# Optimization experiments

Hardware: AMD Instinct MI355X
Metric: run time of the kernel (lower is better)

Reference implementation:

```python
import jax, jax.numpy as jnp
import numpy as np

B, L, D = 8, 8192, 768  # trees, leaves per tree, d_in == d_hidden


def setup_inputs() -> dict:
    key = jax.random.key(0)
    ks = jax.random.split(key, 5)
    scale = 0.02  # keep gates out of saturation
    return {
        "leaf_emb": jax.random.normal(ks[0], (B, L, D), dtype=jnp.float32),
        "W_iou": jax.random.normal(ks[1], (3 * D, D), dtype=jnp.float32) * scale,
        "b_iou": jnp.zeros((3 * D,), dtype=jnp.float32),
        "U_iou": jax.random.normal(ks[2], (3 * D, D), dtype=jnp.float32) * scale,
        "W_f": jax.random.normal(ks[3], (D, D), dtype=jnp.float32) * scale,
        "b_f": jnp.zeros((D,), dtype=jnp.float32),
        "U_f": jax.random.normal(ks[4], (D, D), dtype=jnp.float32) * scale,
    }


def reference(leaf_emb, W_iou, b_iou, U_iou, W_f, b_f, U_f):
    """Child-Sum Tree-LSTM over a perfect binary tree, level-synchronous.

    Leaves: h = embedding, c = 0 (matches the torch module's leaf case).
    Internal node with children (l, r):
      h_sum = h_l + h_r; x = h_sum / 2
      i,o,u = split(W_iou x + b_iou + U_iou h_sum)
      f_k   = sigmoid(W_f x + b_f + U_f h_k)   per child
      c = sigmoid(i)*tanh(u) + f_l*c_l + f_r*c_r;  h = sigmoid(o)*tanh(c)
    Returns stacked (h_root, c_root): [2, B, D].
    """
    h = leaf_emb                      # [B, n, D]
    c = jnp.zeros_like(h)
    while h.shape[1] > 1:             # static trace-time loop over depth (13 levels)
        hl, hr = h[:, 0::2], h[:, 1::2]   # [B, n/2, D]
        cl, cr = c[:, 0::2], c[:, 1::2]
        h_sum = hl + hr
        x = h_sum * 0.5               # x_j = h_sum / num_children (==2)
        iou = jnp.einsum('bnd,gd->bng', x, W_iou) + b_iou \
            + jnp.einsum('bnd,gd->bng', h_sum, U_iou)
        i, o, u = jnp.split(iou, 3, axis=-1)
        wfx = jnp.einsum('bnd,hd->bnh', x, W_f) + b_f
        f_l = jax.nn.sigmoid(wfx + jnp.einsum('bnd,hd->bnh', hl, U_f))
        f_r = jax.nn.sigmoid(wfx + jnp.einsum('bnd,hd->bnh', hr, U_f))
        c = jax.nn.sigmoid(i) * jnp.tanh(u) + f_l * cl + f_r * cr
        h = jax.nn.sigmoid(o) * jnp.tanh(c)
    return jnp.stack([h[:, 0], c[:, 0]])  # [2, B, D]
```

## Files before the change

kernel.cpp:

```cpp
#include <hip/hip_runtime.h>


typedef _Float16 half8 __attribute__((ext_vector_type(8)));
typedef float f32x4 __attribute__((ext_vector_type(4)));

#define ROWB 1536
#define NT 24
#define BUFA 36864
#define BUFT 26624

__device__ __forceinline__ float sigm(float x){ return 1.f/(1.f+__expf(-x)); }
__device__ __forceinline__ float tanhfast(float x){ return 1.f - 2.f/(1.f+__expf(2.f*x)); }

__device__ __forceinline__ void gload16(const void* g, void* l){
  __builtin_amdgcn_global_load_lds((const __attribute__((address_space(1))) void*)g,
                                   (__attribute__((address_space(3))) void*)l, 16, 0, 0);
}

__global__ void prep_weights(const float* __restrict__ Wiou, const float* __restrict__ Uiou,
                             const float* __restrict__ Wf, const float* __restrict__ Uf,
                             _Float16* __restrict__ Bw)
{
    const int n1 = 2304 * 768, n2 = n1 + 589824, n3 = n2 + 589824;
    int stride = gridDim.x * blockDim.x;
    for (int idx = blockIdx.x * blockDim.x + threadIdx.x; idx < n3; idx += stride) {
        float v;
        if (idx < n1)      v = __fmaf_rn(0.5f, Wiou[idx], Uiou[idx]);
        else if (idx < n2) v = 0.5f * Wf[idx - n1];
        else               v = Uf[idx - n2];
        Bw[idx] = (_Float16)v;
    }
}

__global__ void cast_leaves(const float* __restrict__ x, _Float16* __restrict__ h, int n8)
{
    int stride = gridDim.x * blockDim.x;
    for (int i = blockIdx.x * blockDim.x + threadIdx.x; i < n8; i += stride) {
        float4 v0 = ((const float4*)x)[2 * i];
        float4 v1 = ((const float4*)x)[2 * i + 1];
        half8 o = { (_Float16)v0.x, (_Float16)v0.y, (_Float16)v0.z, (_Float16)v0.w,
                    (_Float16)v1.x, (_Float16)v1.y, (_Float16)v1.z, (_Float16)v1.w };
        ((half8*)h)[i] = o;
    }
}

__global__ __launch_bounds__(256, 2) void tree_level(
    const _Float16* __restrict__ Hc, const float* __restrict__ Cc,
    const _Float16* __restrict__ Bw,
    const float* __restrict__ biou, const float* __restrict__ bfv,
    _Float16* __restrict__ Hn, float* __restrict__ Cn,
    int M, int mblocks, int firstLevel)
{
    __shared__ __align__(16) char smem[2 * BUFA];
    const int tid = threadIdx.x;
    const int lane = tid & 63;
    const int w = tid >> 6;
    const int wm = w >> 1;
    const int wd = w & 1;

    const int nwg = mblocks * 12;
    const int orig = blockIdx.x;
    const int xcd = orig & 7, qx = nwg >> 3, rx = nwg & 7;
    const int v = (xcd < rx ? xcd * (qx + 1) : rx * (qx + 1) + (xcd - rx) * qx) + (orig >> 3);
    const int mb = v / 12;
    const int d0c = v - mb * 12;
    const int mBase = mb * 128;
    const int d0 = d0c * 64;

    const int l3 = lane >> 3, j = lane & 7;
    const int jjA = j ^ l3;
    const int rbase = w * 8 + l3;
    unsigned offH[4];
#pragma unroll
    for (int s = 0; s < 4; ++s)
        offH[s] = (unsigned)(2 * (mBase + s * 32 + rbase) + (jjA >> 2)) * ROWB + (jjA & 3) * 16;
    const int pB = w * 8 + l3;
    unsigned offWb[5];
#pragma unroll
    for (int t = 0; t < 5; ++t)
        offWb[t] = (unsigned)(t * 768 + d0 + 2 * pB + (jjA >> 2)) * ROWB + (jjA & 3) * 16;
    const int wK = w * 1024;

#define STAGE_A(bi, ko) do { \
    _Pragma("unroll") for (int s = 0; s < 4; ++s) \
        gload16((const char*)Hc + offH[s] + (ko), smem + (bi) * BUFA + s * 4096 + wK); \
    _Pragma("unroll") for (int t = 0; t < 5; ++t) \
        gload16((const char*)Bw + offWb[t] + (ko), smem + (bi) * BUFA + 16384 + t * 4096 + wK); \
} while (0)

    const int q = lane >> 4;
    const int lr16 = lane & 15;
    int offA[4], offB[2];
#pragma unroll
    for (int fm = 0; fm < 4; ++fm) {
        int r = wm * 64 + fm * 16 + lr16;
        offA[fm] = r * 128 + ((q ^ (r & 7)) * 16);
    }
#pragma unroll
    for (int fd = 0; fd < 2; ++fd) {
        int cl = wd * 32 + fd * 16 + lr16;
        int p = cl >> 1;
        int jb = ((cl & 1) * 4 + q) ^ (p & 7);
        offB[fd] = 16384 + p * 128 + jb * 16;
    }

    f32x4 acc[6][4][2];
#pragma unroll
    for (int g = 0; g < 6; ++g)
#pragma unroll
        for (int a = 0; a < 4; ++a)
#pragma unroll
            for (int b2 = 0; b2 < 2; ++b2)
                acc[g][a][b2] = (f32x4){0.f, 0.f, 0.f, 0.f};

    STAGE_A(0, 0);
    int cur = 0;
    for (int kt = 0; kt < NT; ++kt) {
        if (kt + 1 < NT) {
            STAGE_A(cur ^ 1, (kt + 1) * 64);
            asm volatile("s_waitcnt vmcnt(9)" ::: "memory");
        } else {
            asm volatile("s_waitcnt vmcnt(0)" ::: "memory");
        }
        __builtin_amdgcn_s_barrier();
        __builtin_amdgcn_sched_barrier(0);
        const char* bb = smem + cur * BUFA;
        half8 hl[4], hr[4];
#pragma unroll
        for (int fm = 0; fm < 4; ++fm) {
            hl[fm] = *(const half8*)(bb + offA[fm]);
            hr[fm] = *(const half8*)(bb + (offA[fm] ^ 64));
        }
        __builtin_amdgcn_s_setprio(1);
#pragma unroll
        for (int fd = 0; fd < 2; ++fd) {
            const char* bp = bb + offB[fd];
            half8 b0 = *(const half8*)(bp);
            half8 b1 = *(const half8*)(bp + 4096);
            half8 b2 = *(const half8*)(bp + 8192);
            half8 b3 = *(const half8*)(bp + 12288);
            half8 b4 = *(const half8*)(bp + 16384);
#pragma unroll
            for (int fm = 0; fm < 4; ++fm) {
                acc[4][fm][fd] = __builtin_amdgcn_mfma_f32_16x16x32_f16(hl[fm], b4, acc[4][fm][fd], 0, 0, 0);
                half8 hs = hl[fm] + hr[fm];
                acc[0][fm][fd] = __builtin_amdgcn_mfma_f32_16x16x32_f16(hs, b0, acc[0][fm][fd], 0, 0, 0);
                acc[1][fm][fd] = __builtin_amdgcn_mfma_f32_16x16x32_f16(hs, b1, acc[1][fm][fd], 0, 0, 0);
                acc[2][fm][fd] = __builtin_amdgcn_mfma_f32_16x16x32_f16(hs, b2, acc[2][fm][fd], 0, 0, 0);
                acc[3][fm][fd] = __builtin_amdgcn_mfma_f32_16x16x32_f16(hs, b3, acc[3][fm][fd], 0, 0, 0);
                acc[5][fm][fd] = __builtin_amdgcn_mfma_f32_16x16x32_f16(hs, b4, acc[5][fm][fd], 0, 0, 0);
            }
        }
        __builtin_amdgcn_s_setprio(0);
        if (kt + 1 < NT) __builtin_amdgcn_s_barrier();
        cur ^= 1;
    }

#pragma unroll
    for (int fd = 0; fd < 2; ++fd) {
        const int col = d0 + wd * 32 + fd * 16 + lr16;
        const float bi = biou[col];
        const float bo = biou[768 + col];
        const float bu = biou[1536 + col];
        const float bf = bfv[col];
#pragma unroll
        for (int fm = 0; fm < 4; ++fm) {
            const int rb = mBase + wm * 64 + fm * 16 + q * 4;
#pragma unroll
            for (int r4 = 0; r4 < 4; ++r4) {
                int row = rb + r4;
                float iv = acc[0][fm][fd][r4] + bi;
                float ov = acc[1][fm][fd][r4] + bo;
                float uv = acc[2][fm][fd][r4] + bu;
                float wfx = acc[3][fm][fd][r4] + bf;
                float g6 = acc[4][fm][fd][r4];
                float fl = sigm(wfx + g6);
                float fr = sigm(wfx + acc[5][fm][fd][r4] - g6);
                float clv = 0.f, crv = 0.f;
                if (!firstLevel) {
                    clv = Cc[(size_t)(2 * row) * 768 + col];
                    crv = Cc[(size_t)(2 * row + 1) * 768 + col];
                }
                float c = sigm(iv) * tanhfast(uv) + fl * clv + fr * crv;
                float h = sigm(ov) * tanhfast(c);
                Hn[(size_t)row * 768 + col] = (_Float16)h;
                Cn[(size_t)row * 768 + col] = c;
            }
        }
    }
}

__global__ __launch_bounds__(256, 3) void tree_small(
    const _Float16* __restrict__ Hc, const float* __restrict__ Cc,
    const _Float16* __restrict__ Bw,
    const float* __restrict__ biou, const float* __restrict__ bfv,
    _Float16* __restrict__ Hn, float* __restrict__ Cn,
    float* __restrict__ out,
    int M, int finalLevel)
{
    __shared__ __align__(16) char smem[2 * BUFT];
    const int tid = threadIdx.x;
    const int lane = tid & 63;
    const int w = tid >> 6;
    const int wm = w >> 1;
    const int wd = w & 1;
    const int bid = blockIdx.x;
    const int mb = bid / 24;
    const int d0c = bid - mb * 24;
    const int mBase = mb * 128;
    const int d0 = d0c * 32;

    const int l3 = lane >> 3, j = lane & 7;
    const int jj0 = j ^ l3;

    unsigned offWb[3];
    int dstB[3];
#pragma unroll
    for (int s = 0; s < 3; ++s) {
        int i = s * 4 + w;
        if (i >= 10) i -= 2;
        int t = i >> 1, half = i & 1;
        int p = half * 8 + l3;
        offWb[s] = (unsigned)(t * 768 + d0 + 2 * p + (jj0 >> 2)) * ROWB + (jj0 & 3) * 16;
        dstB[s] = 16384 + t * 2048 + half * 1024;
    }
    unsigned offHa[4];
    int dstA[4];
#pragma unroll
    for (int s = 0; s < 4; ++s) {
        int u = s * 4 + w;
        int gr = mBase + u * 8 + l3;
        if (gr >= M) gr = M - 1;
        offHa[s] = (unsigned)(2 * gr + (jj0 >> 2)) * ROWB + (jj0 & 3) * 16;
        dstA[s] = u * 1024;
    }

#define STAGE_T(bi_, ko) do { \
    _Pragma("unroll") for (int s = 0; s < 4; ++s) \
        gload16((const char*)Hc + offHa[s] + (ko), smem + (bi_) * BUFT + dstA[s]); \
    _Pragma("unroll") for (int s = 0; s < 3; ++s) \
        gload16((const char*)Bw + offWb[s] + (ko), smem + (bi_) * BUFT + dstB[s]); \
} while (0)

    const int q = lane >> 4;
    const int lr16 = lane & 15;
    int offA[4];
#pragma unroll
    for (int fm = 0; fm < 4; ++fm) {
        int r = wm * 64 + fm * 16 + lr16;
        offA[fm] = r * 128 + ((q ^ (r & 7)) * 16);
    }
    int offB;
    {
        int cl = wd * 16 + lr16;
        int p = cl >> 1;
        int jb = ((cl & 1) * 4 + q) ^ (p & 7);
        offB = 16384 + p * 128 + jb * 16;
    }

    f32x4 acc[6][4];
#pragma unroll
    for (int g = 0; g < 6; ++g)
#pragma unroll
        for (int a = 0; a < 4; ++a)
            acc[g][a] = (f32x4){0.f, 0.f, 0.f, 0.f};

    STAGE_T(0, 0);
    int cur = 0;
    for (int kt = 0; kt < NT; ++kt) {
        if (kt + 1 < NT) {
            STAGE_T(cur ^ 1, (kt + 1) * 64);
            asm volatile("s_waitcnt vmcnt(7)" ::: "memory");
        } else {
            asm volatile("s_waitcnt vmcnt(0)" ::: "memory");
        }
        __builtin_amdgcn_s_barrier();
        __builtin_amdgcn_sched_barrier(0);
        const char* bb = smem + cur * BUFT;
        half8 b0 = *(const half8*)(bb + offB);
        half8 b1 = *(const half8*)(bb + offB + 2048);
        half8 b2 = *(const half8*)(bb + offB + 4096);
        half8 b3 = *(const half8*)(bb + offB + 6144);
        half8 b4 = *(const half8*)(bb + offB + 8192);
        __builtin_amdgcn_s_setprio(1);
#pragma unroll
        for (int fm = 0; fm < 4; ++fm) {
            half8 hl = *(const half8*)(bb + offA[fm]);
            half8 hr = *(const half8*)(bb + (offA[fm] ^ 64));
            acc[4][fm] = __builtin_amdgcn_mfma_f32_16x16x32_f16(hl, b4, acc[4][fm], 0, 0, 0);
            half8 hs = hl + hr;
            acc[0][fm] = __builtin_amdgcn_mfma_f32_16x16x32_f16(hs, b0, acc[0][fm], 0, 0, 0);
            acc[1][fm] = __builtin_amdgcn_mfma_f32_16x16x32_f16(hs, b1, acc[1][fm], 0, 0, 0);
            acc[2][fm] = __builtin_amdgcn_mfma_f32_16x16x32_f16(hs, b2, acc[2][fm], 0, 0, 0);
            acc[3][fm] = __builtin_amdgcn_mfma_f32_16x16x32_f16(hs, b3, acc[3][fm], 0, 0, 0);
            acc[5][fm] = __builtin_amdgcn_mfma_f32_16x16x32_f16(hs, b4, acc[5][fm], 0, 0, 0);
        }
        __builtin_amdgcn_s_setprio(0);
        if (kt + 1 < NT) __builtin_amdgcn_s_barrier();
        cur ^= 1;
    }

    const int col = d0 + wd * 16 + lr16;
    const float bi = biou[col];
    const float bo = biou[768 + col];
    const float bu = biou[1536 + col];
    const float bf = bfv[col];
#pragma unroll
    for (int fm = 0; fm < 4; ++fm) {
        const int rb = mBase + wm * 64 + fm * 16 + q * 4;
#pragma unroll
        for (int r4 = 0; r4 < 4; ++r4) {
            int row = rb + r4;
            if (row < M) {
                float iv = acc[0][fm][r4] + bi;
                float ov = acc[1][fm][r4] + bo;
                float uv = acc[2][fm][r4] + bu;
                float wfx = acc[3][fm][r4] + bf;
                float g6 = acc[4][fm][r4];
                float fl = sigm(wfx + g6);
                float fr = sigm(wfx + acc[5][fm][r4] - g6);
                float clv = Cc[(size_t)(2 * row) * 768 + col];
                float crv = Cc[(size_t)(2 * row + 1) * 768 + col];
                float c = sigm(iv) * tanhfast(uv) + fl * clv + fr * crv;
                float h = sigm(ov) * tanhfast(c);
                if (finalLevel) {
                    out[row * 768 + col] = h;
                    out[6144 + row * 768 + col] = c;
                } else {
                    Hn[(size_t)row * 768 + col] = (_Float16)h;
                    Cn[(size_t)row * 768 + col] = c;
                }
            }
        }
    }
}

extern "C" void kernel_launch(void* const* d_in, const int* in_sizes, int n_in,
                              void* d_out, int out_size, void* d_ws, size_t ws_size,
                              hipStream_t stream)
{
    const float* leaf = (const float*)d_in[0];
    const float* Wiou = (const float*)d_in[1];
    const float* biou = (const float*)d_in[2];
    const float* Uiou = (const float*)d_in[3];
    const float* Wf   = (const float*)d_in[4];
    const float* bfv  = (const float*)d_in[5];
    const float* Uf   = (const float*)d_in[6];

    char* ws = (char*)d_ws;
    _Float16* Bw = (_Float16*)(ws);
    _Float16* H0 = (_Float16*)(ws + 5898240);
    _Float16* H1 = (_Float16*)(ws + 106561536);
    float*    C0 = (float*)(ws + 156893184);
    float*    C1 = (float*)(ws + 257556480);

    prep_weights<<<1024, 256, 0, stream>>>(Wiou, Uiou, Wf, Uf, Bw);
    cast_leaves<<<2048, 256, 0, stream>>>(leaf, H0, 50331648 / 8);

    float* out = (float*)d_out;
    _Float16* Hc = H0; _Float16* Hn = H1;
    float* Cc = C1; float* Cn = C0;
    int rows = 65536, level = 0;
    while (rows > 8) {
        int M = rows >> 1;
        if (M >= 4096) {
            int mblocks = M / 128;
            tree_level<<<mblocks * 12, 256, 0, stream>>>(Hc, Cc, Bw, biou, bfv,
                Hn, Cn, M, mblocks, level == 0 ? 1 : 0);
        } else {
            int mblocks = (M + 127) / 128;
            int fin = (M == 8) ? 1 : 0;
            tree_small<<<mblocks * 24, 256, 0, stream>>>(Hc, Cc, Bw, biou, bfv,
                Hn, Cn, out, M, fin);
        }
        _Float16* th = Hc; Hc = Hn; Hn = th;
        float* tc = Cc; Cc = Cn; Cn = tc;
        rows = M; ++level;
    }
}
```

Measured before the change: 1.074 ms.

## Reformulate forget-gate GEMMs and fuse tail levels into persistent grid-synced kernel

The forget-gate weights are re-packed so each child's gate comes out of two MFMAs on hl and hr (0.5Wf+Uf and 0.5Wf) accumulated into one register set. This drops one accumulator group and one sum step in the epilogue, though each k-step now issues seven MFMAs per fragment instead of six. The small levels (M≤2048) now run in a single persistent 256-block kernel that separates levels with a global atomic barrier, replacing the per-level launches. Row bounds guards are also added to the big-level kernel. The persistent kernel relies on all 256 blocks being resident at once, or the spin barrier deadlocks.

```diff
diff --git a/kernel.cpp b/kernel.cpp
--- a/kernel.cpp
+++ b/kernel.cpp
@@ -19,15 +19,16 @@
 
 __global__ void prep_weights(const float* __restrict__ Wiou, const float* __restrict__ Uiou,
                              const float* __restrict__ Wf, const float* __restrict__ Uf,
-                             _Float16* __restrict__ Bw)
+                             _Float16* __restrict__ Bw, unsigned* __restrict__ barCnt)
 {
+    if (blockIdx.x == 0 && threadIdx.x == 0) atomicExch(barCnt, 0u);
     const int n1 = 2304 * 768, n2 = n1 + 589824, n3 = n2 + 589824;
     int stride = gridDim.x * blockDim.x;
     for (int idx = blockIdx.x * blockDim.x + threadIdx.x; idx < n3; idx += stride) {
         float v;
         if (idx < n1)      v = __fmaf_rn(0.5f, Wiou[idx], Uiou[idx]);
-        else if (idx < n2) v = 0.5f * Wf[idx - n1];
-        else               v = Uf[idx - n2];
+        else if (idx < n2) { int k = idx - n1; v = __fmaf_rn(0.5f, Wf[k], Uf[k]); }
+        else               { int k = idx - n2; v = 0.5f * Wf[k]; }
         Bw[idx] = (_Float16)v;
     }
 }
@@ -72,8 +73,11 @@
     const int rbase = w * 8 + l3;
     unsigned offH[4];
 #pragma unroll
-    for (int s = 0; s < 4; ++s)
-        offH[s] = (unsigned)(2 * (mBase + s * 32 + rbase) + (jjA >> 2)) * ROWB + (jjA & 3) * 16;
+    for (int s = 0; s < 4; ++s) {
+        int gr = mBase + s * 32 + rbase;
+        if (gr >= M) gr = M - 1;
+        offH[s] = (unsigned)(2 * gr + (jjA >> 2)) * ROWB + (jjA & 3) * 16;
+    }
     const int pB = w * 8 + l3;
     unsigned offWb[5];
 #pragma unroll
@@ -104,9 +108,9 @@
         offB[fd] = 16384 + p * 128 + jb * 16;
     }
 
-    f32x4 acc[6][4][2];
-#pragma unroll
-    for (int g = 0; g < 6; ++g)
+    f32x4 acc[5][4][2];
+#pragma unroll
+    for (int g = 0; g < 5; ++g)
 #pragma unroll
         for (int a = 0; a < 4; ++a)
 #pragma unroll
@@ -142,13 +146,14 @@
             half8 b4 = *(const half8*)(bp + 16384);
 #pragma unroll
             for (int fm = 0; fm < 4; ++fm) {
-                acc[4][fm][fd] = __builtin_amdgcn_mfma_f32_16x16x32_f16(hl[fm], b4, acc[4][fm][fd], 0, 0, 0);
                 half8 hs = hl[fm] + hr[fm];
                 acc[0][fm][fd] = __builtin_amdgcn_mfma_f32_16x16x32_f16(hs, b0, acc[0][fm][fd], 0, 0, 0);
                 acc[1][fm][fd] = __builtin_amdgcn_mfma_f32_16x16x32_f16(hs, b1, acc[1][fm][fd], 0, 0, 0);
                 acc[2][fm][fd] = __builtin_amdgcn_mfma_f32_16x16x32_f16(hs, b2, acc[2][fm][fd], 0, 0, 0);
-                acc[3][fm][fd] = __builtin_amdgcn_mfma_f32_16x16x32_f16(hs, b3, acc[3][fm][fd], 0, 0, 0);
-                acc[5][fm][fd] = __builtin_amdgcn_mfma_f32_16x16x32_f16(hs, b4, acc[5][fm][fd], 0, 0, 0);
+                acc[3][fm][fd] = __builtin_amdgcn_mfma_f32_16x16x32_f16(hl[fm], b3, acc[3][fm][fd], 0, 0, 0);
+                acc[3][fm][fd] = __builtin_amdgcn_mfma_f32_16x16x32_f16(hr[fm], b4, acc[3][fm][fd], 0, 0, 0);
+                acc[4][fm][fd] = __builtin_amdgcn_mfma_f32_16x16x32_f16(hl[fm], b4, acc[4][fm][fd], 0, 0, 0);
+                acc[4][fm][fd] = __builtin_amdgcn_mfma_f32_16x16x32_f16(hr[fm], b3, acc[4][fm][fd], 0, 0, 0);
             }
         }
         __builtin_amdgcn_s_setprio(0);
@@ -169,34 +174,33 @@
 #pragma unroll
             for (int r4 = 0; r4 < 4; ++r4) {
                 int row = rb + r4;
-                float iv = acc[0][fm][fd][r4] + bi;
-                float ov = acc[1][fm][fd][r4] + bo;
-                float uv = acc[2][fm][fd][r4] + bu;
-                float wfx = acc[3][fm][fd][r4] + bf;
-                float g6 = acc[4][fm][fd][r4];
-                float fl = sigm(wfx + g6);
-                float fr = sigm(wfx + acc[5][fm][fd][r4] - g6);
-                float clv = 0.f, crv = 0.f;
-                if (!firstLevel) {
-                    clv = Cc[(size_t)(2 * row) * 768 + col];
-                    crv = Cc[(size_t)(2 * row + 1) * 768 + col];
+                if (row < M) {
+                    float iv = acc[0][fm][fd][r4] + bi;
+                    float ov = acc[1][fm][fd][r4] + bo;
+                    float uv = acc[2][fm][fd][r4] + bu;
+                    float fl = sigm(acc[3][fm][fd][r4] + bf);
+                    float fr = sigm(acc[4][fm][fd][r4] + bf);
+                    float clv = 0.f, crv = 0.f;
+                    if (!firstLevel) {
+                        clv = Cc[(size_t)(2 * row) * 768 + col];
+                        crv = Cc[(size_t)(2 * row + 1) * 768 + col];
+                    }
+                    float c = sigm(iv) * tanhfast(uv) + fl * clv + fr * crv;
+                    float h = sigm(ov) * tanhfast(c);
+                    Hn[(size_t)row * 768 + col] = (_Float16)h;
+                    Cn[(size_t)row * 768 + col] = c;
                 }
-                float c = sigm(iv) * tanhfast(uv) + fl * clv + fr * crv;
-                float h = sigm(ov) * tanhfast(c);
-                Hn[(size_t)row * 768 + col] = (_Float16)h;
-                Cn[(size_t)row * 768 + col] = c;
-            }
-        }
-    }
-}
-
-__global__ __launch_bounds__(256, 3) void tree_small(
-    const _Float16* __restrict__ Hc, const float* __restrict__ Cc,
+            }
+        }
+    }
+}
+
+__global__ __launch_bounds__(256) void tree_tail(
     const _Float16* __restrict__ Bw,
     const float* __restrict__ biou, const float* __restrict__ bfv,
-    _Float16* __restrict__ Hn, float* __restrict__ Cn,
-    float* __restrict__ out,
-    int M, int finalLevel)
+    _Float16* __restrict__ HcIn, _Float16* __restrict__ HnIn,
+    float* __restrict__ CcIn, float* __restrict__ CnIn,
+    float* __restrict__ out, unsigned* __restrict__ barCnt)
 {
     __shared__ __align__(16) char smem[2 * BUFT];
     const int tid = threadIdx.x;
@@ -204,46 +208,24 @@
     const int w = tid >> 6;
     const int wm = w >> 1;
     const int wd = w & 1;
-    const int bid = blockIdx.x;
-    const int mb = bid / 24;
-    const int d0c = bid - mb * 24;
-    const int mBase = mb * 128;
-    const int d0 = d0c * 32;
-
     const int l3 = lane >> 3, j = lane & 7;
     const int jj0 = j ^ l3;
-
-    unsigned offWb[3];
-    int dstB[3];
+    const int q = lane >> 4;
+    const int lr16 = lane & 15;
+
+    int dstA[4];
+#pragma unroll
+    for (int s = 0; s < 4; ++s) dstA[s] = (s * 4 + w) * 1024;
+    int colW[3], dstB[3];
 #pragma unroll
     for (int s = 0; s < 3; ++s) {
         int i = s * 4 + w;
         if (i >= 10) i -= 2;
         int t = i >> 1, half = i & 1;
         int p = half * 8 + l3;
-        offWb[s] = (unsigned)(t * 768 + d0 + 2 * p + (jj0 >> 2)) * ROWB + (jj0 & 3) * 16;
+        colW[s] = t * 768 + 2 * p + (jj0 >> 2);
         dstB[s] = 16384 + t * 2048 + half * 1024;
     }
-    unsigned offHa[4];
-    int dstA[4];
-#pragma unroll
-    for (int s = 0; s < 4; ++s) {
-        int u = s * 4 + w;
-        int gr = mBase + u * 8 + l3;
-        if (gr >= M) gr = M - 1;
-        offHa[s] = (unsigned)(2 * gr + (jj0 >> 2)) * ROWB + (jj0 & 3) * 16;
-        dstA[s] = u * 1024;
-    }
-
-#define STAGE_T(bi_, ko) do { \
-    _Pragma("unroll") for (int s = 0; s < 4; ++s) \
-        gload16((const char*)Hc + offHa[s] + (ko), smem + (bi_) * BUFT + dstA[s]); \
-    _Pragma("unroll") for (int s = 0; s < 3; ++s) \
-        gload16((const char*)Bw + offWb[s] + (ko), smem + (bi_) * BUFT + dstB[s]); \
-} while (0)
-
-    const int q = lane >> 4;
-    const int lr16 = lane & 15;
     int offA[4];
 #pragma unroll
     for (int fm = 0; fm < 4; ++fm) {
@@ -258,79 +240,129 @@
         offB = 16384 + p * 128 + jb * 16;
     }
 
-    f32x4 acc[6][4];
-#pragma unroll
-    for (int g = 0; g < 6; ++g)
-#pragma unroll
-        for (int a = 0; a < 4; ++a)
-            acc[g][a] = (f32x4){0.f, 0.f, 0.f, 0.f};
-
-    STAGE_T(0, 0);
-    int cur = 0;
-    for (int kt = 0; kt < NT; ++kt) {
-        if (kt + 1 < NT) {
-            STAGE_T(cur ^ 1, (kt + 1) * 64);
-            asm volatile("s_waitcnt vmcnt(7)" ::: "memory");
-        } else {
-            asm volatile("s_waitcnt vmcnt(0)" ::: "memory");
-        }
-        __builtin_amdgcn_s_barrier();
-        __builtin_amdgcn_sched_barrier(0);
-        const char* bb = smem + cur * BUFT;
-        half8 b0 = *(const half8*)(bb + offB);
-        half8 b1 = *(const half8*)(bb + offB + 2048);
-        half8 b2 = *(const half8*)(bb + offB + 4096);
-        half8 b3 = *(const half8*)(bb + offB + 6144);
-        half8 b4 = *(const half8*)(bb + offB + 8192);
-        __builtin_amdgcn_s_setprio(1);
-#pragma unroll
-        for (int fm = 0; fm < 4; ++fm) {
-            half8 hl = *(const half8*)(bb + offA[fm]);
-            half8 hr = *(const half8*)(bb + (offA[fm] ^ 64));
-            acc[4][fm] = __builtin_amdgcn_mfma_f32_16x16x32_f16(hl, b4, acc[4][fm], 0, 0, 0);
-            half8 hs = hl + hr;
-            acc[0][fm] = __builtin_amdgcn_mfma_f32_16x16x32_f16(hs, b0, acc[0][fm], 0, 0, 0);
-            acc[1][fm] = __builtin_amdgcn_mfma_f32_16x16x32_f16(hs, b1, acc[1][fm], 0, 0, 0);
-            acc[2][fm] = __builtin_amdgcn_mfma_f32_16x16x32_f16(hs, b2, acc[2][fm], 0, 0, 0);
-            acc[3][fm] = __builtin_amdgcn_mfma_f32_16x16x32_f16(hs, b3, acc[3][fm], 0, 0, 0);
-            acc[5][fm] = __builtin_amdgcn_mfma_f32_16x16x32_f16(hs, b4, acc[5][fm], 0, 0, 0);
-        }
-        __builtin_amdgcn_s_setprio(0);
-        if (kt + 1 < NT) __builtin_amdgcn_s_barrier();
-        cur ^= 1;
-    }
-
-    const int col = d0 + wd * 16 + lr16;
-    const float bi = biou[col];
-    const float bo = biou[768 + col];
-    const float bu = biou[1536 + col];
-    const float bf = bfv[col];
-#pragma unroll
-    for (int fm = 0; fm < 4; ++fm) {
-        const int rb = mBase + wm * 64 + fm * 16 + q * 4;
-#pragma unroll
-        for (int r4 = 0; r4 < 4; ++r4) {
-            int row = rb + r4;
-            if (row < M) {
-                float iv = acc[0][fm][r4] + bi;
-                float ov = acc[1][fm][r4] + bo;
-                float uv = acc[2][fm][r4] + bu;
-                float wfx = acc[3][fm][r4] + bf;
-                float g6 = acc[4][fm][r4];
-                float fl = sigm(wfx + g6);
-                float fr = sigm(wfx + acc[5][fm][r4] - g6);
-                float clv = Cc[(size_t)(2 * row) * 768 + col];
-                float crv = Cc[(size_t)(2 * row + 1) * 768 + col];
-                float c = sigm(iv) * tanhfast(uv) + fl * clv + fr * crv;
-                float h = sigm(ov) * tanhfast(c);
-                if (finalLevel) {
-                    out[row * 768 + col] = h;
-                    out[6144 + row * 768 + col] = c;
+    const _Float16* hc = HcIn; _Float16* hn = HnIn;
+    const float* cc = CcIn;    float* cn = CnIn;
+    unsigned target = 0;
+
+    for (int M = 2048; M >= 8; M >>= 1) {
+        const int mblocks = (M + 127) >> 7;
+        const int nact = mblocks * 24;
+        for (int t = blockIdx.x; t < nact; t += 256) {
+            __syncthreads();
+            const int mb = t / 24;
+            const int d0c = t - mb * 24;
+            const int mBase = mb * 128;
+            const int d0 = d0c * 32;
+
+            unsigned offHa_[4];
+#pragma unroll
+            for (int s = 0; s < 4; ++s) {
+                int gr = mBase + (s * 4 + w) * 8 + l3;
+                if (gr >= M) gr = M - 1;
+                offHa_[s] = (unsigned)(2 * gr + (jj0 >> 2)) * ROWB + (jj0 & 3) * 16;
+            }
+            unsigned offWb_[3];
+#pragma unroll
+            for (int s = 0; s < 3; ++s)
+                offWb_[s] = (unsigned)(colW[s] + d0) * ROWB + (jj0 & 3) * 16;
+
+#define STAGE_T(bi_, ko) do { \
+    _Pragma("unroll") for (int s = 0; s < 4; ++s) \
+        gload16((const char*)hc + offHa_[s] + (ko), smem + (bi_) * BUFT + dstA[s]); \
+    _Pragma("unroll") for (int s = 0; s < 3; ++s) \
+        gload16((const char*)Bw + offWb_[s] + (ko), smem + (bi_) * BUFT + dstB[s]); \
+} while (0)
+
+            f32x4 acc[5][4];
+#pragma unroll
+            for (int g = 0; g < 5; ++g)
+#pragma unroll
+                for (int a = 0; a < 4; ++a)
+                    acc[g][a] = (f32x4){0.f, 0.f, 0.f, 0.f};
+
+            STAGE_T(0, 0);
+            int cur = 0;
+            for (int kt = 0; kt < NT; ++kt) {
+                if (kt + 1 < NT) {
+                    STAGE_T(cur ^ 1, (kt + 1) * 64);
+                    asm volatile("s_waitcnt vmcnt(7)" ::: "memory");
                 } else {
-                    Hn[(size_t)row * 768 + col] = (_Float16)h;
-                    Cn[(size_t)row * 768 + col] = c;
+                    asm volatile("s_waitcnt vmcnt(0)" ::: "memory");
                 }
-            }
+                __builtin_amdgcn_s_barrier();
+                __builtin_amdgcn_sched_barrier(0);
+                const char* bb = smem + cur * BUFT;
+                half8 b0 = *(const half8*)(bb + offB);
+                half8 b1 = *(const half8*)(bb + offB + 2048);
+                half8 b2 = *(const half8*)(bb + offB + 4096);
+                half8 b3 = *(const half8*)(bb + offB + 6144);
+                half8 b4 = *(const half8*)(bb + offB + 8192);
+                __builtin_amdgcn_s_setprio(1);
+#pragma unroll
+                for (int fm = 0; fm < 4; ++fm) {
+                    half8 hl = *(const half8*)(bb + offA[fm]);
+                    half8 hr = *(const half8*)(bb + (offA[fm] ^ 64));
+                    acc[3][fm] = __builtin_amdgcn_mfma_f32_16x16x32_f16(hl, b3, acc[3][fm], 0, 0, 0);
+                    acc[4][fm] = __builtin_amdgcn_mfma_f32_16x16x32_f16(hl, b4, acc[4][fm], 0, 0, 0);
+                    half8 hs = hl + hr;
+                    acc[0][fm] = __builtin_amdgcn_mfma_f32_16x16x32_f16(hs, b0, acc[0][fm], 0, 0, 0);
+                    acc[1][fm] = __builtin_amdgcn_mfma_f32_16x16x32_f16(hs, b1, acc[1][fm], 0, 0, 0);
+                    acc[2][fm] = __builtin_amdgcn_mfma_f32_16x16x32_f16(hs, b2, acc[2][fm], 0, 0, 0);
+                    acc[3][fm] = __builtin_amdgcn_mfma_f32_16x16x32_f16(hr, b4, acc[3][fm], 0, 0, 0);
+                    acc[4][fm] = __builtin_amdgcn_mfma_f32_16x16x32_f16(hr, b3, acc[4][fm], 0, 0, 0);
+                }
+                __builtin_amdgcn_s_setprio(0);
+                if (kt + 1 < NT) __builtin_amdgcn_s_barrier();
+                cur ^= 1;
+            }
+
+            const int col = d0 + wd * 16 + lr16;
+            const float bi = biou[col];
+            const float bo = biou[768 + col];
+            const float bu = biou[1536 + col];
+            const float bf = bfv[col];
+            const int fin = (M == 8);
+#pragma unroll
+            for (int fm = 0; fm < 4; ++fm) {
+                const int rb = mBase + wm * 64 + fm * 16 + q * 4;
+#pragma unroll
+                for (int r4 = 0; r4 < 4; ++r4) {
+                    int row = rb + r4;
+                    if (row < M) {
+                        float iv = acc[0][fm][r4] + bi;
+                        float ov = acc[1][fm][r4] + bo;
+                        float uv = acc[2][fm][r4] + bu;
+                        float fl = sigm(acc[3][fm][r4] + bf);
+                        float fr = sigm(acc[4][fm][r4] + bf);
+                        float clv = cc[(size_t)(2 * row) * 768 + col];
+                        float crv = cc[(size_t)(2 * row + 1) * 768 + col];
+                        float c = sigm(iv) * tanhfast(uv) + fl * clv + fr * crv;
+                        float h = sigm(ov) * tanhfast(c);
+                        if (fin) {
+                            out[row * 768 + col] = h;
+                            out[6144 + row * 768 + col] = c;
+                        } else {
+                            hn[(size_t)row * 768 + col] = (_Float16)h;
+                            cn[(size_t)row * 768 + col] = c;
+                        }
+                    }
+                }
+            }
+        }
+
+        if (M > 8) {
+            __threadfence();
+            __syncthreads();
+            if (tid == 0) {
+                target += 256;
+                __hip_atomic_fetch_add(barCnt, 1u, __ATOMIC_RELEASE, __HIP_MEMORY_SCOPE_AGENT);
+                while (__hip_atomic_load(barCnt, __ATOMIC_ACQUIRE, __HIP_MEMORY_SCOPE_AGENT) < target)
+                    __builtin_amdgcn_s_sleep(2);
+            }
+            __syncthreads();
+            __threadfence();
+            const _Float16* th = hc; hc = hn; hn = (_Float16*)th;
+            const float* tc = cc; cc = cn; cn = (float*)tc;
         }
     }
 }
@@ -348,33 +380,28 @@
     const float* Uf   = (const float*)d_in[6];
 
     char* ws = (char*)d_ws;
-    _Float16* Bw = (_Float16*)(ws);
-    _Float16* H0 = (_Float16*)(ws + 5898240);
-    _Float16* H1 = (_Float16*)(ws + 106561536);
-    float*    C0 = (float*)(ws + 156893184);
-    float*    C1 = (float*)(ws + 257556480);
-
-    prep_weights<<<1024, 256, 0, stream>>>(Wiou, Uiou, Wf, Uf, Bw);
+    _Float16* Bw  = (_Float16*)(ws);
+    unsigned* cnt = (unsigned*)(ws + 5898240);
+    _Float16* H0  = (_Float16*)(ws + 5898496);
+    _Float16* H1  = (_Float16*)(ws + 106561792);
+    float*    C0  = (float*)(ws + 156893440);
+    float*    C1  = (float*)(ws + 257556736);
+
+    prep_weights<<<1024, 256, 0, stream>>>(Wiou, Uiou, Wf, Uf, Bw, cnt);
     cast_leaves<<<2048, 256, 0, stream>>>(leaf, H0, 50331648 / 8);
 
     float* out = (float*)d_out;
     _Float16* Hc = H0; _Float16* Hn = H1;
     float* Cc = C1; float* Cn = C0;
     int rows = 65536, level = 0;
-    while (rows > 8) {
+    while (rows > 4096) {
         int M = rows >> 1;
-        if (M >= 4096) {
-            int mblocks = M / 128;
-            tree_level<<<mblocks * 12, 256, 0, stream>>>(Hc, Cc, Bw, biou, bfv,
-                Hn, Cn, M, mblocks, level == 0 ? 1 : 0);
-        } else {
-            int mblocks = (M + 127) / 128;
-            int fin = (M == 8) ? 1 : 0;
-            tree_small<<<mblocks * 24, 256, 0, stream>>>(Hc, Cc, Bw, biou, bfv,
-                Hn, Cn, out, M, fin);
-        }
+        int mblocks = M / 128;
+        tree_level<<<mblocks * 12, 256, 0, stream>>>(Hc, Cc, Bw, biou, bfv,
+            Hn, Cn, M, mblocks, level == 0 ? 1 : 0);
         _Float16* th = Hc; Hc = Hn; Hn = th;
         float* tc = Cc; Cc = Cn; Cn = tc;
         rows = M; ++level;
     }
-}
+    tree_tail<<<256, 256, 0, stream>>>(Bw, biou, bfv, Hc, Hn, Cc, Cn, out, cnt);
+}
```

New measurement: 2.094 ms. 1.95x slower.

## Load weight fragments directly from global, refactor forget-gate GEMM algebra

Applied to the files above, without the earlier changes.

Weight B-fragments are now read straight from global memory (L2-resident) into registers instead of being staged through LDS, which shrinks the LDS buffers and staging work per k-step. The forget-gate math is restructured so that W_f/2+U_f and W_f/2 are applied to h_l and h_r separately, producing f_l and f_r pre-activations directly and dropping one accumulator set (6 to 5), at the cost of 7 MFMAs per fragment instead of 6. Row clamping and row<M guards are added to the large kernel. Global loads inside the compute loop add latency that is no longer hidden by the LDS double-buffering pipeline.

```diff
diff --git a/kernel.cpp b/kernel.cpp
--- a/kernel.cpp
+++ b/kernel.cpp
@@ -6,8 +6,9 @@
 
 #define ROWB 1536
 #define NT 24
-#define BUFA 36864
-#define BUFT 26624
+#define MATB 1179648
+#define BUFA 16384
+#define BUFT 16384
 
 __device__ __forceinline__ float sigm(float x){ return 1.f/(1.f+__expf(-x)); }
 __device__ __forceinline__ float tanhfast(float x){ return 1.f - 2.f/(1.f+__expf(2.f*x)); }
@@ -26,8 +27,8 @@
     for (int idx = blockIdx.x * blockDim.x + threadIdx.x; idx < n3; idx += stride) {
         float v;
         if (idx < n1)      v = __fmaf_rn(0.5f, Wiou[idx], Uiou[idx]);
-        else if (idx < n2) v = 0.5f * Wf[idx - n1];
-        else               v = Uf[idx - n2];
+        else if (idx < n2) { int k = idx - n1; v = __fmaf_rn(0.5f, Wf[k], Uf[k]); }
+        else               { int k = idx - n2; v = 0.5f * Wf[k]; }
         Bw[idx] = (_Float16)v;
     }
 }
@@ -72,41 +73,36 @@
     const int rbase = w * 8 + l3;
     unsigned offH[4];
 #pragma unroll
-    for (int s = 0; s < 4; ++s)
-        offH[s] = (unsigned)(2 * (mBase + s * 32 + rbase) + (jjA >> 2)) * ROWB + (jjA & 3) * 16;
-    const int pB = w * 8 + l3;
-    unsigned offWb[5];
-#pragma unroll
-    for (int t = 0; t < 5; ++t)
-        offWb[t] = (unsigned)(t * 768 + d0 + 2 * pB + (jjA >> 2)) * ROWB + (jjA & 3) * 16;
+    for (int s = 0; s < 4; ++s) {
+        int gr = mBase + s * 32 + rbase;
+        if (gr >= M) gr = M - 1;
+        offH[s] = (unsigned)(2 * gr + (jjA >> 2)) * ROWB + (jjA & 3) * 16;
+    }
     const int wK = w * 1024;
 
 #define STAGE_A(bi, ko) do { \
     _Pragma("unroll") for (int s = 0; s < 4; ++s) \
         gload16((const char*)Hc + offH[s] + (ko), smem + (bi) * BUFA + s * 4096 + wK); \
-    _Pragma("unroll") for (int t = 0; t < 5; ++t) \
-        gload16((const char*)Bw + offWb[t] + (ko), smem + (bi) * BUFA + 16384 + t * 4096 + wK); \
 } while (0)
 
     const int q = lane >> 4;
     const int lr16 = lane & 15;
-    int offA[4], offB[2];
+    int offA[4];
 #pragma unroll
     for (int fm = 0; fm < 4; ++fm) {
         int r = wm * 64 + fm * 16 + lr16;
         offA[fm] = r * 128 + ((q ^ (r & 7)) * 16);
     }
+    size_t offBg[2];
 #pragma unroll
     for (int fd = 0; fd < 2; ++fd) {
-        int cl = wd * 32 + fd * 16 + lr16;
-        int p = cl >> 1;
-        int jb = ((cl & 1) * 4 + q) ^ (p & 7);
-        offB[fd] = 16384 + p * 128 + jb * 16;
-    }
-
-    f32x4 acc[6][4][2];
-#pragma unroll
-    for (int g = 0; g < 6; ++g)
+        int colOut = d0 + wd * 32 + fd * 16 + lr16;
+        offBg[fd] = (size_t)colOut * ROWB + q * 16;
+    }
+
+    f32x4 acc[5][4][2];
+#pragma unroll
+    for (int g = 0; g < 5; ++g)
 #pragma unroll
         for (int a = 0; a < 4; ++a)
 #pragma unroll
@@ -118,37 +114,34 @@
     for (int kt = 0; kt < NT; ++kt) {
         if (kt + 1 < NT) {
             STAGE_A(cur ^ 1, (kt + 1) * 64);
-            asm volatile("s_waitcnt vmcnt(9)" ::: "memory");
+            asm volatile("s_waitcnt vmcnt(4)" ::: "memory");
         } else {
             asm volatile("s_waitcnt vmcnt(0)" ::: "memory");
         }
         __builtin_amdgcn_s_barrier();
         __builtin_amdgcn_sched_barrier(0);
         const char* bb = smem + cur * BUFA;
-        half8 hl[4], hr[4];
+        half8 b[2][5];
+#pragma unroll
+        for (int fd = 0; fd < 2; ++fd)
+#pragma unroll
+            for (int t = 0; t < 5; ++t)
+                b[fd][t] = *(const half8*)((const char*)Bw + (size_t)t * MATB + offBg[fd] + kt * 64);
+        __builtin_amdgcn_s_setprio(1);
 #pragma unroll
         for (int fm = 0; fm < 4; ++fm) {
-            hl[fm] = *(const half8*)(bb + offA[fm]);
-            hr[fm] = *(const half8*)(bb + (offA[fm] ^ 64));
-        }
-        __builtin_amdgcn_s_setprio(1);
-#pragma unroll
-        for (int fd = 0; fd < 2; ++fd) {
-            const char* bp = bb + offB[fd];
-            half8 b0 = *(const half8*)(bp);
-            half8 b1 = *(const half8*)(bp + 4096);
-            half8 b2 = *(const half8*)(bp + 8192);
-            half8 b3 = *(const half8*)(bp + 12288);
-            half8 b4 = *(const half8*)(bp + 16384);
-#pragma unroll
-            for (int fm = 0; fm < 4; ++fm) {
-                acc[4][fm][fd] = __builtin_amdgcn_mfma_f32_16x16x32_f16(hl[fm], b4, acc[4][fm][fd], 0, 0, 0);
-                half8 hs = hl[fm] + hr[fm];
-                acc[0][fm][fd] = __builtin_amdgcn_mfma_f32_16x16x32_f16(hs, b0, acc[0][fm][fd], 0, 0, 0);
-                acc[1][fm][fd] = __builtin_amdgcn_mfma_f32_16x16x32_f16(hs, b1, acc[1][fm][fd], 0, 0, 0);
-                acc[2][fm][fd] = __builtin_amdgcn_mfma_f32_16x16x32_f16(hs, b2, acc[2][fm][fd], 0, 0, 0);
-                acc[3][fm][fd] = __builtin_amdgcn_mfma_f32_16x16x32_f16(hs, b3, acc[3][fm][fd], 0, 0, 0);
-                acc[5][fm][fd] = __builtin_amdgcn_mfma_f32_16x16x32_f16(hs, b4, acc[5][fm][fd], 0, 0, 0);
+            half8 hl = *(const half8*)(bb + offA[fm]);
+            half8 hr = *(const half8*)(bb + (offA[fm] ^ 64));
+            half8 hs = hl + hr;
+#pragma unroll
+            for (int fd = 0; fd < 2; ++fd) {
+                acc[0][fm][fd] = __builtin_amdgcn_mfma_f32_16x16x32_f16(hs, b[fd][0], acc[0][fm][fd], 0, 0, 0);
+                acc[1][fm][fd] = __builtin_amdgcn_mfma_f32_16x16x32_f16(hs, b[fd][1], acc[1][fm][fd], 0, 0, 0);
+                acc[2][fm][fd] = __builtin_amdgcn_mfma_f32_16x16x32_f16(hs, b[fd][2], acc[2][fm][fd], 0, 0, 0);
+                acc[3][fm][fd] = __builtin_amdgcn_mfma_f32_16x16x32_f16(hl, b[fd][3], acc[3][fm][fd], 0, 0, 0);
+                acc[3][fm][fd] = __builtin_amdgcn_mfma_f32_16x16x32_f16(hr, b[fd][4], acc[3][fm][fd], 0, 0, 0);
+                acc[4][fm][fd] = __builtin_amdgcn_mfma_f32_16x16x32_f16(hl, b[fd][4], acc[4][fm][fd], 0, 0, 0);
+                acc[4][fm][fd] = __builtin_amdgcn_mfma_f32_16x16x32_f16(hr, b[fd][3], acc[4][fm][fd], 0, 0, 0);
             }
         }
         __builtin_amdgcn_s_setprio(0);
@@ -169,22 +162,22 @@
 #pragma unroll
             for (int r4 = 0; r4 < 4; ++r4) {
                 int row = rb + r4;
-                float iv = acc[0][fm][fd][r4] + bi;
-                float ov = acc[1][fm][fd][r4] + bo;
-                float uv = acc[2][fm][fd][r4] + bu;
-                float wfx = acc[3][fm][fd][r4] + bf;
-                float g6 = acc[4][fm][fd][r4];
-                float fl = sigm(wfx + g6);
-                float fr = sigm(wfx + acc[5][fm][fd][r4] - g6);
-                float clv = 0.f, crv = 0.f;
-                if (!firstLevel) {
-                    clv = Cc[(size_t)(2 * row) * 768 + col];
-                    crv = Cc[(size_t)(2 * row + 1) * 768 + col];
+                if (row < M) {
+                    float iv = acc[0][fm][fd][r4] + bi;
+                    float ov = acc[1][fm][fd][r4] + bo;
+                    float uv = acc[2][fm][fd][r4] + bu;
+                    float fl = sigm(acc[3][fm][fd][r4] + bf);
+                    float fr = sigm(acc[4][fm][fd][r4] + bf);
+                    float clv = 0.f, crv = 0.f;
+                    if (!firstLevel) {
+                        clv = Cc[(size_t)(2 * row) * 768 + col];
+                        crv = Cc[(size_t)(2 * row + 1) * 768 + col];
+                    }
+                    float c = sigm(iv) * tanhfast(uv) + fl * clv + fr * crv;
+                    float h = sigm(ov) * tanhfast(c);
+                    Hn[(size_t)row * 768 + col] = (_Float16)h;
+                    Cn[(size_t)row * 768 + col] = c;
                 }
-                float c = sigm(iv) * tanhfast(uv) + fl * clv + fr * crv;
-                float h = sigm(ov) * tanhfast(c);
-                Hn[(size_t)row * 768 + col] = (_Float16)h;
-                Cn[(size_t)row * 768 + col] = c;
             }
         }
     }
@@ -213,17 +206,6 @@
     const int l3 = lane >> 3, j = lane & 7;
     const int jj0 = j ^ l3;
 
-    unsigned offWb[3];
-    int dstB[3];
-#pragma unroll
-    for (int s = 0; s < 3; ++s) {
-        int i = s * 4 + w;
-        if (i >= 10) i -= 2;
-        int t = i >> 1, half = i & 1;
-        int p = half * 8 + l3;
-        offWb[s] = (unsigned)(t * 768 + d0 + 2 * p + (jj0 >> 2)) * ROWB + (jj0 & 3) * 16;
-        dstB[s] = 16384 + t * 2048 + half * 1024;
-    }
     unsigned offHa[4];
     int dstA[4];
 #pragma unroll
@@ -238,8 +220,6 @@
 #define STAGE_T(bi_, ko) do { \
     _Pragma("unroll") for (int s = 0; s < 4; ++s) \
         gload16((const char*)Hc + offHa[s] + (ko), smem + (bi_) * BUFT + dstA[s]); \
-    _Pragma("unroll") for (int s = 0; s < 3; ++s) \
-        gload16((const char*)Bw + offWb[s] + (ko), smem + (bi_) * BUFT + dstB[s]); \
 } while (0)
 
     const int q = lane >> 4;
@@ -250,17 +230,12 @@
         int r = wm * 64 + fm * 16 + lr16;
         offA[fm] = r * 128 + ((q ^ (r & 7)) * 16);
     }
-    int offB;
-    {
-        int cl = wd * 16 + lr16;
-        int p = cl >> 1;
-        int jb = ((cl & 1) * 4 + q) ^ (p & 7);
-        offB = 16384 + p * 128 + jb * 16;
-    }
-
-    f32x4 acc[6][4];
-#pragma unroll
-    for (int g = 0; g < 6; ++g)
+    const int colOut = d0 + wd * 16 + lr16;
+    const size_t offBg = (size_t)colOut * ROWB + q * 16;
+
+    f32x4 acc[5][4];
+#pragma unroll
+    for (int g = 0; g < 5; ++g)
 #pragma unroll
         for (int a = 0; a < 4; ++a)
             acc[g][a] = (f32x4){0.f, 0.f, 0.f, 0.f};
@@ -270,41 +245,41 @@
     for (int kt = 0; kt < NT; ++kt) {
         if (kt + 1 < NT) {
             STAGE_T(cur ^ 1, (kt + 1) * 64);
-            asm volatile("s_waitcnt vmcnt(7)" ::: "memory");
+            asm volatile("s_waitcnt vmcnt(4)" ::: "memory");
         } else {
             asm volatile("s_waitcnt vmcnt(0)" ::: "memory");
         }
         __builtin_amdgcn_s_barrier();
         __builtin_amdgcn_sched_barrier(0);
         const char* bb = smem + cur * BUFT;
-        half8 b0 = *(const half8*)(bb + offB);
-        half8 b1 = *(const half8*)(bb + offB + 2048);
-        half8 b2 = *(const half8*)(bb + offB + 4096);
-        half8 b3 = *(const half8*)(bb + offB + 6144);
-        half8 b4 = *(const half8*)(bb + offB + 8192);
+        half8 b0 = *(const half8*)((const char*)Bw + 0 * (size_t)MATB + offBg + kt * 64);
+        half8 b1 = *(const half8*)((const char*)Bw + 1 * (size_t)MATB + offBg + kt * 64);
+        half8 b2 = *(const half8*)((const char*)Bw + 2 * (size_t)MATB + offBg + kt * 64);
+        half8 b3 = *(const half8*)((const char*)Bw + 3 * (size_t)MATB + offBg + kt * 64);
+        half8 b4 = *(const half8*)((const char*)Bw + 4 * (size_t)MATB + offBg + kt * 64);
         __builtin_amdgcn_s_setprio(1);
 #pragma unroll
         for (int fm = 0; fm < 4; ++fm) {
             half8 hl = *(const half8*)(bb + offA[fm]);
             half8 hr = *(const half8*)(bb + (offA[fm] ^ 64));
+            acc[3][fm] = __builtin_amdgcn_mfma_f32_16x16x32_f16(hl, b3, acc[3][fm], 0, 0, 0);
             acc[4][fm] = __builtin_amdgcn_mfma_f32_16x16x32_f16(hl, b4, acc[4][fm], 0, 0, 0);
             half8 hs = hl + hr;
             acc[0][fm] = __builtin_amdgcn_mfma_f32_16x16x32_f16(hs, b0, acc[0][fm], 0, 0, 0);
             acc[1][fm] = __builtin_amdgcn_mfma_f32_16x16x32_f16(hs, b1, acc[1][fm], 0, 0, 0);
             acc[2][fm] = __builtin_amdgcn_mfma_f32_16x16x32_f16(hs, b2, acc[2][fm], 0, 0, 0);
-            acc[3][fm] = __builtin_amdgcn_mfma_f32_16x16x32_f16(hs, b3, acc[3][fm], 0, 0, 0);
-            acc[5][fm] = __builtin_amdgcn_mfma_f32_16x16x32_f16(hs, b4, acc[5][fm], 0, 0, 0);
+            acc[3][fm] = __builtin_amdgcn_mfma_f32_16x16x32_f16(hr, b4, acc[3][fm], 0, 0, 0);
+            acc[4][fm] = __builtin_amdgcn_mfma_f32_16x16x32_f16(hr, b3, acc[4][fm], 0, 0, 0);
         }
         __builtin_amdgcn_s_setprio(0);
         if (kt + 1 < NT) __builtin_amdgcn_s_barrier();
         cur ^= 1;
     }
 
-    const int col = d0 + wd * 16 + lr16;
-    const float bi = biou[col];
-    const float bo = biou[768 + col];
-    const float bu = biou[1536 + col];
-    const float bf = bfv[col];
+    const float bi = biou[colOut];
+    const float bo = biou[768 + colOut];
+    const float bu = biou[1536 + colOut];
+    const float bf = bfv[colOut];
 #pragma unroll
     for (int fm = 0; fm < 4; ++fm) {
         const int rb = mBase + wm * 64 + fm * 16 + q * 4;
@@ -315,20 +290,18 @@
                 float iv = acc[0][fm][r4] + bi;
                 float ov = acc[1][fm][r4] + bo;
                 float uv = acc[2][fm][r4] + bu;
-                float wfx = acc[3][fm][r4] + bf;
-                float g6 = acc[4][fm][r4];
-                float fl = sigm(wfx + g6);
-                float fr = sigm(wfx + acc[5][fm][r4] - g6);
-                float clv = Cc[(size_t)(2 * row) * 768 + col];
-                float crv = Cc[(size_t)(2 * row + 1) * 768 + col];
+                float fl = sigm(acc[3][fm][r4] + bf);
+                float fr = sigm(acc[4][fm][r4] + bf);
+                float clv = Cc[(size_t)(2 * row) * 768 + colOut];
+                float crv = Cc[(size_t)(2 * row + 1) * 768 + colOut];
                 float c = sigm(iv) * tanhfast(uv) + fl * clv + fr * crv;
                 float h = sigm(ov) * tanhfast(c);
                 if (finalLevel) {
-                    out[row * 768 + col] = h;
-                    out[6144 + row * 768 + col] = c;
+                    out[row * 768 + colOut] = h;
+                    out[6144 + row * 768 + colOut] = c;
                 } else {
-                    Hn[(size_t)row * 768 + col] = (_Float16)h;
-                    Cn[(size_t)row * 768 + col] = c;
+                    Hn[(size_t)row * 768 + colOut] = (_Float16)h;
+                    Cn[(size_t)row * 768 + colOut] = c;
                 }
             }
         }
```

Measured after the change: 1.384 ms. 1.29x slower.
